# Kernel tuning notes

Measured on AMD Instinct MI355X. Metric: run time of the kernel, lower is better.

Reference implementation:

```python
import jax, jax.numpy as jnp
import numpy as np

B, T, I, H = 256, 2048, 12, 64


def setup_inputs() -> dict:
    key = jax.random.key(0)
    ks = jax.random.split(key, 7)
    s_ih = 1.0 / np.sqrt(H)
    return {
        "x": jax.random.normal(ks[0], (B, T, I), dtype=jnp.float32),
        "w_ih": jax.random.uniform(ks[1], (4 * H, I), minval=-s_ih, maxval=s_ih, dtype=jnp.float32),
        "w_hh": jax.random.uniform(ks[2], (4 * H, H), minval=-s_ih, maxval=s_ih, dtype=jnp.float32),
        "b_ih": jax.random.uniform(ks[3], (4 * H,), minval=-s_ih, maxval=s_ih, dtype=jnp.float32),
        "b_hh": jax.random.uniform(ks[4], (4 * H,), minval=-s_ih, maxval=s_ih, dtype=jnp.float32),
        "fc_w": jax.random.uniform(ks[5], (1, H), minval=-s_ih, maxval=s_ih, dtype=jnp.float32),
        "fc_b": jax.random.uniform(ks[6], (1,), minval=-s_ih, maxval=s_ih, dtype=jnp.float32),
    }


def _lstm(x, w_ih, w_hh, b_ih, b_hh):
    # Precompute input projections for all timesteps: [B,T,4H]
    gx = jnp.einsum("bti,gi->btg", x, w_ih) + b_ih + b_hh
    gx = jnp.swapaxes(gx, 0, 1)  # [T,B,4H] for scan over time
    h0 = jnp.zeros((x.shape[0], w_hh.shape[1]), dtype=x.dtype)
    c0 = jnp.zeros_like(h0)
    Hd = w_hh.shape[1]

    def step(carry, g_t):
        h, c = carry
        gates = g_t + h @ w_hh.T  # [B,4H]
        i = jax.nn.sigmoid(gates[:, 0 * Hd:1 * Hd])
        f = jax.nn.sigmoid(gates[:, 1 * Hd:2 * Hd])
        g = jnp.tanh(gates[:, 2 * Hd:3 * Hd])
        o = jax.nn.sigmoid(gates[:, 3 * Hd:4 * Hd])
        c_new = f * c + i * g
        h_new = o * jnp.tanh(c_new)
        return (h_new, c_new), h_new

    _, hs = jax.lax.scan(step, (h0, c0), gx)  # hs: [T,B,H]
    return jnp.swapaxes(hs, 0, 1)  # [B,T,H]


def reference(x, w_ih, w_hh, b_ih, b_hh, fc_w, fc_b):
    out = _lstm(x, w_ih, w_hh, b_ih, b_hh)            # [B,T,H]
    return jnp.einsum("bth,oh->bto", out, fc_w) + fc_b  # [B,T,1]
```

## Files before the change

### kernel.cpp

```cpp
#include <hip/hip_runtime.h>

constexpr int Bn = 256;
constexpr int Tn = 2048;
constexpr int In = 12;
constexpr int Hn = 64;
constexpr int TCH = 512;
constexpr int CHUNK = 16;

constexpr float LOG2E = 1.44269504088896340736f;

__device__ __forceinline__ float frcp(float v) { return __builtin_amdgcn_rcpf(v); }

template <int CTRL>
__device__ __forceinline__ float dppq(float v) {
    int i = __float_as_int(v);
    i = __builtin_amdgcn_mov_dpp(i, CTRL, 0xF, 0xF, false);
    return __int_as_float(i);
}
__device__ __forceinline__ float rdl(float v, int l) {
    return __int_as_float(__builtin_amdgcn_readlane(__float_as_int(v), l));
}

extern "C" __global__ void __launch_bounds__(256, 1)
lstm_fused_kernel(const float* __restrict__ x,
                  const float* __restrict__ w_ih,
                  const float* __restrict__ w_hh,
                  const float* __restrict__ b_ih,
                  const float* __restrict__ b_hh,
                  const float* __restrict__ fc_w,
                  const float* __restrict__ fc_b,
                  float* __restrict__ out)
{
    __shared__ __align__(16) float xbuf[TCH * 16];
    __shared__ __align__(16) float pbuf[2][4][256];
    __shared__ __align__(16) float hist[CHUNK][Hn];

    const int tid  = threadIdx.x;
    const int lane = tid & 63;
    const int w    = tid >> 6;
    const int g    = lane & 3;
    const int i16  = lane >> 2;
    const int jown = 16 * w + i16;
    const int ro   = 64 * g + jown;
    const int b    = blockIdx.x;

    const int wbase = ((lane >> 2) & 3) * 64 + (lane >> 4) * 16 + 4 * (lane & 3);
    const int rbase = w * 64 + g * 16 + i16;

    const float4* xsrc4 = (const float4*)(x + (size_t)b * Tn * In);

    #pragma unroll
    for (int k = 0; k < 8; ++k) {
        int idx = tid + k * 256;
        xbuf[(idx >> 2) * 16 + 12 + (idx & 3)] = 0.0f;
    }

    float whh_s[4][16];
    #pragma unroll
    for (int r = 0; r < 4; ++r) {
        const float4* src = (const float4*)(w_hh + (4 * lane + r) * Hn + 16 * w);
        float4 v0 = src[0], v1 = src[1], v2 = src[2], v3 = src[3];
        whh_s[r][0]=v0.x;  whh_s[r][1]=v0.y;  whh_s[r][2]=v0.z;  whh_s[r][3]=v0.w;
        whh_s[r][4]=v1.x;  whh_s[r][5]=v1.y;  whh_s[r][6]=v1.z;  whh_s[r][7]=v1.w;
        whh_s[r][8]=v2.x;  whh_s[r][9]=v2.y;  whh_s[r][10]=v2.z; whh_s[r][11]=v2.w;
        whh_s[r][12]=v3.x; whh_s[r][13]=v3.y; whh_s[r][14]=v3.z; whh_s[r][15]=v3.w;
    }
    #pragma unroll
    for (int r = 0; r < 4; ++r)
        #pragma unroll
        for (int k = 0; k < 16; k += 4)
            asm volatile("" : "+v"(whh_s[r][k+0]), "+v"(whh_s[r][k+1]),
                              "+v"(whh_s[r][k+2]), "+v"(whh_s[r][k+3]));

    float wih_s[4][4];
    if (w < 3) {
        #pragma unroll
        for (int r = 0; r < 4; ++r) {
            float4 v = *(const float4*)(w_ih + (4 * lane + r) * In + 4 * w);
            wih_s[r][0]=v.x; wih_s[r][1]=v.y; wih_s[r][2]=v.z; wih_s[r][3]=v.w;
        }
    } else {
        #pragma unroll
        for (int r = 0; r < 4; ++r)
            wih_s[r][0]=wih_s[r][1]=wih_s[r][2]=wih_s[r][3]=0.0f;
    }
    #pragma unroll
    for (int r = 0; r < 4; ++r)
        asm volatile("" : "+v"(wih_s[r][0]), "+v"(wih_s[r][1]),
                          "+v"(wih_s[r][2]), "+v"(wih_s[r][3]));

    const float bias = b_ih[ro] + b_hh[ro];
    const float m    = (g == 2) ? 2.0f : 1.0f;
    const float madd = (g == 2) ? -1.0f : 0.0f;
    const float me   = (g == 2) ? (-2.0f * LOG2E) : (-LOG2E);
    const int   fq   = tid & 15;
    const int   fs   = tid >> 4;
    const float4 fw4 = *(const float4*)(fc_w + 4 * fq);
    const float fcb  = fc_b[0];

    float h_own = 0.0f;
    float c     = 0.0f;

    float* outb = out + (size_t)b * Tn;

    for (int ci = 0; ci < Tn / CHUNK; ++ci) {
        const int T0 = ci * CHUNK;

        if ((T0 & (TCH - 1)) == 0) {
            const int qtr = T0 >> 9;
            #pragma unroll
            for (int k = 0; k < 6; ++k) {
                int li  = tid + k * 256;
                int t_l = li / 3;
                int i4  = li % 3;
                ((float4*)xbuf)[t_l * 4 + i4] = xsrc4[qtr * 1536 + li];
            }
            __syncthreads();
        }

        #pragma unroll
        for (int s = 0; s < CHUNK; ++s) {
            const int tl = (T0 + s) & (TCH - 1);

            float hs0  = rdl(h_own,  0), hs1  = rdl(h_own,  4);
            float hs2  = rdl(h_own,  8), hs3  = rdl(h_own, 12);
            float hs4  = rdl(h_own, 16), hs5  = rdl(h_own, 20);
            float hs6  = rdl(h_own, 24), hs7  = rdl(h_own, 28);
            float hs8  = rdl(h_own, 32), hs9  = rdl(h_own, 36);
            float hs10 = rdl(h_own, 40), hs11 = rdl(h_own, 44);
            float hs12 = rdl(h_own, 48), hs13 = rdl(h_own, 52);
            float hs14 = rdl(h_own, 56), hs15 = rdl(h_own, 60);

            const float4 xv = *(const float4*)(xbuf + tl * 16 + 4 * w);
            float p0 = hs0 * whh_s[0][0], p1 = hs0 * whh_s[1][0];
            float p2 = hs0 * whh_s[2][0], p3 = hs0 * whh_s[3][0];
            #define HFMA(K, HS) \
                p0 = fmaf(HS, whh_s[0][K], p0);  p1 = fmaf(HS, whh_s[1][K], p1); \
                p2 = fmaf(HS, whh_s[2][K], p2);  p3 = fmaf(HS, whh_s[3][K], p3);
            HFMA(1,  hs1)  HFMA(2,  hs2)  HFMA(3,  hs3)
            HFMA(4,  hs4)  HFMA(5,  hs5)  HFMA(6,  hs6)  HFMA(7,  hs7)
            HFMA(8,  hs8)  HFMA(9,  hs9)  HFMA(10, hs10) HFMA(11, hs11)
            HFMA(12, hs12) HFMA(13, hs13) HFMA(14, hs14) HFMA(15, hs15)
            #undef HFMA
            p0 = fmaf(xv.x, wih_s[0][0], p0);  p1 = fmaf(xv.x, wih_s[1][0], p1);
            p2 = fmaf(xv.x, wih_s[2][0], p2);  p3 = fmaf(xv.x, wih_s[3][0], p3);
            p0 = fmaf(xv.y, wih_s[0][1], p0);  p1 = fmaf(xv.y, wih_s[1][1], p1);
            p2 = fmaf(xv.y, wih_s[2][1], p2);  p3 = fmaf(xv.y, wih_s[3][1], p3);
            p0 = fmaf(xv.z, wih_s[0][2], p0);  p1 = fmaf(xv.z, wih_s[1][2], p1);
            p2 = fmaf(xv.z, wih_s[2][2], p2);  p3 = fmaf(xv.z, wih_s[3][2], p3);
            p0 = fmaf(xv.w, wih_s[0][3], p0);  p1 = fmaf(xv.w, wih_s[1][3], p1);
            p2 = fmaf(xv.w, wih_s[2][3], p2);  p3 = fmaf(xv.w, wih_s[3][3], p3);

            float4 pv; pv.x = p0; pv.y = p1; pv.z = p2; pv.w = p3;
            *(float4*)(&pbuf[s & 1][w][wbase]) = pv;
            __syncthreads();

            const float* pb = &pbuf[s & 1][0][0];
            float a = ((pb[rbase] + pb[256 + rbase]) +
                       (pb[512 + rbase] + pb[768 + rbase])) + bias;
            float e   = exp2f(me * a);
            float act = fmaf(m, frcp(1.0f + e), madd);

            float iv = dppq<0x00>(act);
            float fv = dppq<0x55>(act);
            float gv = dppq<0xAA>(act);
            float ov = dppq<0xFF>(act);

            c = fmaf(fv, c, iv * gv);
            float e2 = exp2f(-2.0f * LOG2E * c);
            h_own = ov * fmaf(2.0f, frcp(1.0f + e2), -1.0f);

            if (g == 0) hist[s][jown] = h_own;
        }

        __syncthreads();
        {
            const float4 hv = *(const float4*)(&hist[fs][4 * fq]);
            float pp = hv.x * fw4.x + hv.y * fw4.y + hv.z * fw4.z + hv.w * fw4.w;
            #pragma unroll
            for (int off = 8; off; off >>= 1)
                pp += __shfl_xor(pp, off, 16);
            if (fq == 0) outb[T0 + fs] = pp + fcb;
        }
    }
}

extern "C" void kernel_launch(void* const* d_in, const int* in_sizes, int n_in,
                              void* d_out, int out_size, void* d_ws, size_t ws_size,
                              hipStream_t stream) {
    const float* x    = (const float*)d_in[0];
    const float* w_ih = (const float*)d_in[1];
    const float* w_hh = (const float*)d_in[2];
    const float* b_ih = (const float*)d_in[3];
    const float* b_hh = (const float*)d_in[4];
    const float* fc_w = (const float*)d_in[5];
    const float* fc_b = (const float*)d_in[6];
    float* out = (float*)d_out;

    lstm_fused_kernel<<<Bn, 256, 0, stream>>>(x, w_ih, w_hh, b_ih, b_hh,
                                              fc_w, fc_b, out);
}
```

Measured before the change: 713.9 us.

## Split LSTM recurrent matvec across eight waves with 512-thread blocks

Doubles the block size to 512 threads, so each of the eight waves handles an 8-column slice of the hidden state instead of a 16-column slice. This halves the per-step readlane broadcasts and the FMA chain on the serial recurrence path. In exchange, the cross-wave reduction now sums eight partials instead of four, using a padded shared buffer. The per-step barrier also spans eight waves, and half of each wave's lanes redundantly compute the gate activations.

```diff
diff --git a/kernel.cpp b/kernel.cpp
--- a/kernel.cpp
+++ b/kernel.cpp
@@ -21,7 +21,7 @@
     return __int_as_float(__builtin_amdgcn_readlane(__float_as_int(v), l));
 }
 
-extern "C" __global__ void __launch_bounds__(256, 1)
+extern "C" __global__ void __launch_bounds__(512, 1)
 lstm_fused_kernel(const float* __restrict__ x,
                   const float* __restrict__ w_ih,
                   const float* __restrict__ w_hh,
@@ -32,69 +32,62 @@
                   float* __restrict__ out)
 {
     __shared__ __align__(16) float xbuf[TCH * 16];
-    __shared__ __align__(16) float pbuf[2][4][256];
+    __shared__ __align__(16) float pbuf[2][8][288];
     __shared__ __align__(16) float hist[CHUNK][Hn];
 
     const int tid  = threadIdx.x;
     const int lane = tid & 63;
     const int w    = tid >> 6;
-    const int g    = lane & 3;
-    const int i16  = lane >> 2;
-    const int jown = 16 * w + i16;
+    const int lh   = lane & 31;
+    const int g    = lh & 3;
+    const int i8   = lh >> 2;
+    const int jown = 8 * w + i8;
     const int ro   = 64 * g + jown;
     const int b    = blockIdx.x;
 
-    const int wbase = ((lane >> 2) & 3) * 64 + (lane >> 4) * 16 + 4 * (lane & 3);
-    const int rbase = w * 64 + g * 16 + i16;
-
     const float4* xsrc4 = (const float4*)(x + (size_t)b * Tn * In);
 
+    {
+        float4 z; z.x = z.y = z.z = z.w = 0.0f;
+        ((float4*)xbuf)[tid * 4 + 3] = z;
+    }
+
+    float whh_s[4][8];
     #pragma unroll
-    for (int k = 0; k < 8; ++k) {
-        int idx = tid + k * 256;
-        xbuf[(idx >> 2) * 16 + 12 + (idx & 3)] = 0.0f;
-    }
-
-    float whh_s[4][16];
+    for (int mm = 0; mm < 4; ++mm) {
+        const float4* src = (const float4*)(w_hh + (64 * mm + lane) * Hn + 8 * w);
+        float4 v0 = src[0], v1 = src[1];
+        whh_s[mm][0]=v0.x; whh_s[mm][1]=v0.y; whh_s[mm][2]=v0.z; whh_s[mm][3]=v0.w;
+        whh_s[mm][4]=v1.x; whh_s[mm][5]=v1.y; whh_s[mm][6]=v1.z; whh_s[mm][7]=v1.w;
+    }
     #pragma unroll
-    for (int r = 0; r < 4; ++r) {
-        const float4* src = (const float4*)(w_hh + (4 * lane + r) * Hn + 16 * w);
-        float4 v0 = src[0], v1 = src[1], v2 = src[2], v3 = src[3];
-        whh_s[r][0]=v0.x;  whh_s[r][1]=v0.y;  whh_s[r][2]=v0.z;  whh_s[r][3]=v0.w;
-        whh_s[r][4]=v1.x;  whh_s[r][5]=v1.y;  whh_s[r][6]=v1.z;  whh_s[r][7]=v1.w;
-        whh_s[r][8]=v2.x;  whh_s[r][9]=v2.y;  whh_s[r][10]=v2.z; whh_s[r][11]=v2.w;
-        whh_s[r][12]=v3.x; whh_s[r][13]=v3.y; whh_s[r][14]=v3.z; whh_s[r][15]=v3.w;
+    for (int mm = 0; mm < 4; ++mm)
+        #pragma unroll
+        for (int k = 0; k < 8; k += 4)
+            asm volatile("" : "+v"(whh_s[mm][k+0]), "+v"(whh_s[mm][k+1]),
+                              "+v"(whh_s[mm][k+2]), "+v"(whh_s[mm][k+3]));
+
+    float wih_s[4][2];
+    if (w < 6) {
+        #pragma unroll
+        for (int mm = 0; mm < 4; ++mm) {
+            float2 v = *(const float2*)(w_ih + (64 * mm + lane) * In + 2 * w);
+            wih_s[mm][0] = v.x; wih_s[mm][1] = v.y;
+        }
+    } else {
+        #pragma unroll
+        for (int mm = 0; mm < 4; ++mm) { wih_s[mm][0] = 0.0f; wih_s[mm][1] = 0.0f; }
     }
     #pragma unroll
-    for (int r = 0; r < 4; ++r)
-        #pragma unroll
-        for (int k = 0; k < 16; k += 4)
-            asm volatile("" : "+v"(whh_s[r][k+0]), "+v"(whh_s[r][k+1]),
-                              "+v"(whh_s[r][k+2]), "+v"(whh_s[r][k+3]));
-
-    float wih_s[4][4];
-    if (w < 3) {
-        #pragma unroll
-        for (int r = 0; r < 4; ++r) {
-            float4 v = *(const float4*)(w_ih + (4 * lane + r) * In + 4 * w);
-            wih_s[r][0]=v.x; wih_s[r][1]=v.y; wih_s[r][2]=v.z; wih_s[r][3]=v.w;
-        }
-    } else {
-        #pragma unroll
-        for (int r = 0; r < 4; ++r)
-            wih_s[r][0]=wih_s[r][1]=wih_s[r][2]=wih_s[r][3]=0.0f;
-    }
-    #pragma unroll
-    for (int r = 0; r < 4; ++r)
-        asm volatile("" : "+v"(wih_s[r][0]), "+v"(wih_s[r][1]),
-                          "+v"(wih_s[r][2]), "+v"(wih_s[r][3]));
+    for (int mm = 0; mm < 4; ++mm)
+        asm volatile("" : "+v"(wih_s[mm][0]), "+v"(wih_s[mm][1]));
 
     const float bias = b_ih[ro] + b_hh[ro];
-    const float m    = (g == 2) ? 2.0f : 1.0f;
-    const float madd = (g == 2) ? -1.0f : 0.0f;
+    const float scl  = (g == 2) ? 2.0f : 1.0f;
+    const float soff = (g == 2) ? -1.0f : 0.0f;
     const float me   = (g == 2) ? (-2.0f * LOG2E) : (-LOG2E);
     const int   fq   = tid & 15;
-    const int   fs   = tid >> 4;
+    const int   fs   = (tid >> 4) & 15;
     const float4 fw4 = *(const float4*)(fc_w + 4 * fq);
     const float fcb  = fc_b[0];
 
@@ -109,8 +102,8 @@
         if ((T0 & (TCH - 1)) == 0) {
             const int qtr = T0 >> 9;
             #pragma unroll
-            for (int k = 0; k < 6; ++k) {
-                int li  = tid + k * 256;
+            for (int k = 0; k < 3; ++k) {
+                int li  = tid + k * 512;
                 int t_l = li / 3;
                 int i4  = li % 3;
                 ((float4*)xbuf)[t_l * 4 + i4] = xsrc4[qtr * 1536 + li];
@@ -122,59 +115,66 @@
         for (int s = 0; s < CHUNK; ++s) {
             const int tl = (T0 + s) & (TCH - 1);
 
-            float hs0  = rdl(h_own,  0), hs1  = rdl(h_own,  4);
-            float hs2  = rdl(h_own,  8), hs3  = rdl(h_own, 12);
-            float hs4  = rdl(h_own, 16), hs5  = rdl(h_own, 20);
-            float hs6  = rdl(h_own, 24), hs7  = rdl(h_own, 28);
-            float hs8  = rdl(h_own, 32), hs9  = rdl(h_own, 36);
-            float hs10 = rdl(h_own, 40), hs11 = rdl(h_own, 44);
-            float hs12 = rdl(h_own, 48), hs13 = rdl(h_own, 52);
-            float hs14 = rdl(h_own, 56), hs15 = rdl(h_own, 60);
-
-            const float4 xv = *(const float4*)(xbuf + tl * 16 + 4 * w);
+            float2 xv;
+            xv.x = 0.0f; xv.y = 0.0f;
+            if (w < 6) xv = *(const float2*)(xbuf + tl * 16 + 2 * w);
+
+            float hs0 = rdl(h_own,  0), hs1 = rdl(h_own,  4);
+            float hs2 = rdl(h_own,  8), hs3 = rdl(h_own, 12);
+            float hs4 = rdl(h_own, 16), hs5 = rdl(h_own, 20);
+            float hs6 = rdl(h_own, 24), hs7 = rdl(h_own, 28);
+
             float p0 = hs0 * whh_s[0][0], p1 = hs0 * whh_s[1][0];
             float p2 = hs0 * whh_s[2][0], p3 = hs0 * whh_s[3][0];
             #define HFMA(K, HS) \
                 p0 = fmaf(HS, whh_s[0][K], p0);  p1 = fmaf(HS, whh_s[1][K], p1); \
                 p2 = fmaf(HS, whh_s[2][K], p2);  p3 = fmaf(HS, whh_s[3][K], p3);
-            HFMA(1,  hs1)  HFMA(2,  hs2)  HFMA(3,  hs3)
-            HFMA(4,  hs4)  HFMA(5,  hs5)  HFMA(6,  hs6)  HFMA(7,  hs7)
-            HFMA(8,  hs8)  HFMA(9,  hs9)  HFMA(10, hs10) HFMA(11, hs11)
-            HFMA(12, hs12) HFMA(13, hs13) HFMA(14, hs14) HFMA(15, hs15)
+            HFMA(1, hs1) HFMA(2, hs2) HFMA(3, hs3)
+            HFMA(4, hs4) HFMA(5, hs5) HFMA(6, hs6) HFMA(7, hs7)
             #undef HFMA
-            p0 = fmaf(xv.x, wih_s[0][0], p0);  p1 = fmaf(xv.x, wih_s[1][0], p1);
-            p2 = fmaf(xv.x, wih_s[2][0], p2);  p3 = fmaf(xv.x, wih_s[3][0], p3);
-            p0 = fmaf(xv.y, wih_s[0][1], p0);  p1 = fmaf(xv.y, wih_s[1][1], p1);
-            p2 = fmaf(xv.y, wih_s[2][1], p2);  p3 = fmaf(xv.y, wih_s[3][1], p3);
-            p0 = fmaf(xv.z, wih_s[0][2], p0);  p1 = fmaf(xv.z, wih_s[1][2], p1);
-            p2 = fmaf(xv.z, wih_s[2][2], p2);  p3 = fmaf(xv.z, wih_s[3][2], p3);
-            p0 = fmaf(xv.w, wih_s[0][3], p0);  p1 = fmaf(xv.w, wih_s[1][3], p1);
-            p2 = fmaf(xv.w, wih_s[2][3], p2);  p3 = fmaf(xv.w, wih_s[3][3], p3);
-
-            float4 pv; pv.x = p0; pv.y = p1; pv.z = p2; pv.w = p3;
-            *(float4*)(&pbuf[s & 1][w][wbase]) = pv;
+            if (w < 6) {
+                p0 = fmaf(xv.x, wih_s[0][0], p0);  p1 = fmaf(xv.x, wih_s[1][0], p1);
+                p2 = fmaf(xv.x, wih_s[2][0], p2);  p3 = fmaf(xv.x, wih_s[3][0], p3);
+                p0 = fmaf(xv.y, wih_s[0][1], p0);  p1 = fmaf(xv.y, wih_s[1][1], p1);
+                p2 = fmaf(xv.y, wih_s[2][1], p2);  p3 = fmaf(xv.y, wih_s[3][1], p3);
+            }
+
+            {
+                float* pw = &pbuf[s & 1][w][0];
+                pw[lane]       = p0;
+                pw[72 + lane]  = p1;
+                pw[144 + lane] = p2;
+                pw[216 + lane] = p3;
+            }
             __syncthreads();
 
-            const float* pb = &pbuf[s & 1][0][0];
-            float a = ((pb[rbase] + pb[256 + rbase]) +
-                       (pb[512 + rbase] + pb[768 + rbase])) + bias;
-            float e   = exp2f(me * a);
-            float act = fmaf(m, frcp(1.0f + e), madd);
-
-            float iv = dppq<0x00>(act);
-            float fv = dppq<0x55>(act);
-            float gv = dppq<0xAA>(act);
-            float ov = dppq<0xFF>(act);
-
-            c = fmaf(fv, c, iv * gv);
-            float e2 = exp2f(-2.0f * LOG2E * c);
-            h_own = ov * fmaf(2.0f, frcp(1.0f + e2), -1.0f);
-
-            if (g == 0) hist[s][jown] = h_own;
+            {
+                const float* pr = &pbuf[s & 1][0][0];
+                const int rb = 72 * g + jown;
+                float q0 = pr[rb],            q1 = pr[288  + rb];
+                float q2 = pr[576 + rb],      q3 = pr[864  + rb];
+                float q4 = pr[1152 + rb],     q5 = pr[1440 + rb];
+                float q6 = pr[1728 + rb],     q7 = pr[2016 + rb];
+                float a = (((q0 + q1) + (q2 + q3)) + ((q4 + q5) + (q6 + q7))) + bias;
+
+                float e   = exp2f(me * a);
+                float act = fmaf(scl, frcp(1.0f + e), soff);
+
+                float iv = dppq<0x00>(act);
+                float fv = dppq<0x55>(act);
+                float gv = dppq<0xAA>(act);
+                float ov = dppq<0xFF>(act);
+
+                c = fmaf(fv, c, iv * gv);
+                float e2 = exp2f(-2.0f * LOG2E * c);
+                h_own = ov * fmaf(2.0f, frcp(1.0f + e2), -1.0f);
+
+                if (g == 0 && lane < 32) hist[s][jown] = h_own;
+            }
         }
 
         __syncthreads();
-        {
+        if (tid < 256) {
             const float4 hv = *(const float4*)(&hist[fs][4 * fq]);
             float pp = hv.x * fw4.x + hv.y * fw4.y + hv.z * fw4.z + hv.w * fw4.w;
             #pragma unroll
@@ -197,6 +197,6 @@
     const float* fc_b = (const float*)d_in[6];
     float* out = (float*)d_out;
 
-    lstm_fused_kernel<<<Bn, 256, 0, stream>>>(x, w_ih, w_hh, b_ih, b_hh,
+    lstm_fused_kernel<<<Bn, 512, 0, stream>>>(x, w_ih, w_hh, b_ih, b_hh,
                                               fc_w, fc_b, out);
 }
```

New measurement: 840.0 us. 1.18x slower.

## Pack two batch chains per 512-thread block with shared barriers

Applied to the files above, without the earlier changes.

Each block now runs two independent LSTM batch chains (512 threads), halving the grid to 128 blocks. Each chain gets its own slice of x, partial-sum and history buffers, and the x staging tile shrinks to 256 timesteps. The intent is to interleave two latency-bound recurrences on one compute unit to hide step latency. The risk is that half the CUs sit idle and every per-step barrier now synchronizes twice as many waves.

```diff
diff --git a/kernel.cpp b/kernel.cpp
--- a/kernel.cpp
+++ b/kernel.cpp
@@ -4,8 +4,12 @@
 constexpr int Tn = 2048;
 constexpr int In = 12;
 constexpr int Hn = 64;
-constexpr int TCH = 512;
+constexpr int TCH = 256;
 constexpr int CHUNK = 16;
+
+constexpr int XBUF = TCH * 16;
+constexpr int PBUF = 2 * 4 * 256;
+constexpr int HIST = CHUNK * Hn;
 
 constexpr float LOG2E = 1.44269504088896340736f;
 
@@ -21,7 +25,7 @@
     return __int_as_float(__builtin_amdgcn_readlane(__float_as_int(v), l));
 }
 
-extern "C" __global__ void __launch_bounds__(256, 1)
+extern "C" __global__ void __launch_bounds__(512, 1)
 lstm_fused_kernel(const float* __restrict__ x,
                   const float* __restrict__ w_ih,
                   const float* __restrict__ w_hh,
@@ -31,29 +35,31 @@
                   const float* __restrict__ fc_b,
                   float* __restrict__ out)
 {
-    __shared__ __align__(16) float xbuf[TCH * 16];
-    __shared__ __align__(16) float pbuf[2][4][256];
-    __shared__ __align__(16) float hist[CHUNK][Hn];
-
-    const int tid  = threadIdx.x;
-    const int lane = tid & 63;
-    const int w    = tid >> 6;
-    const int g    = lane & 3;
-    const int i16  = lane >> 2;
-    const int jown = 16 * w + i16;
-    const int ro   = 64 * g + jown;
-    const int b    = blockIdx.x;
+    __shared__ __align__(16) float xbuf[2 * XBUF];
+    __shared__ __align__(16) float pbuf[2 * PBUF];
+    __shared__ __align__(16) float hist[2 * HIST];
+
+    const int tid   = threadIdx.x;
+    const int chain = tid >> 8;
+    const int lt    = tid & 255;
+    const int lane  = lt & 63;
+    const int w     = lt >> 6;
+    const int g     = lane & 3;
+    const int i16   = lane >> 2;
+    const int jown  = 16 * w + i16;
+    const int ro    = 64 * g + jown;
+    const int b     = 2 * blockIdx.x + chain;
 
     const int wbase = ((lane >> 2) & 3) * 64 + (lane >> 4) * 16 + 4 * (lane & 3);
     const int rbase = w * 64 + g * 16 + i16;
 
+    float* xb  = xbuf + chain * XBUF;
+    float* pb2 = pbuf + chain * PBUF;
+    float* hb  = hist + chain * HIST;
+
     const float4* xsrc4 = (const float4*)(x + (size_t)b * Tn * In);
 
-    #pragma unroll
-    for (int k = 0; k < 8; ++k) {
-        int idx = tid + k * 256;
-        xbuf[(idx >> 2) * 16 + 12 + (idx & 3)] = 0.0f;
-    }
+    ((float4*)xb)[lt * 4 + 3] = float4{0.f, 0.f, 0.f, 0.f};
 
     float whh_s[4][16];
     #pragma unroll
@@ -90,11 +96,11 @@
                           "+v"(wih_s[r][2]), "+v"(wih_s[r][3]));
 
     const float bias = b_ih[ro] + b_hh[ro];
-    const float m    = (g == 2) ? 2.0f : 1.0f;
-    const float madd = (g == 2) ? -1.0f : 0.0f;
+    const float scl  = (g == 2) ? 2.0f : 1.0f;
+    const float soff = (g == 2) ? -1.0f : 0.0f;
     const float me   = (g == 2) ? (-2.0f * LOG2E) : (-LOG2E);
-    const int   fq   = tid & 15;
-    const int   fs   = tid >> 4;
+    const int   fq   = lt & 15;
+    const int   fs   = lt >> 4;
     const float4 fw4 = *(const float4*)(fc_w + 4 * fq);
     const float fcb  = fc_b[0];
 
@@ -107,13 +113,13 @@
         const int T0 = ci * CHUNK;
 
         if ((T0 & (TCH - 1)) == 0) {
-            const int qtr = T0 >> 9;
+            const int qtr = T0 >> 8;
             #pragma unroll
-            for (int k = 0; k < 6; ++k) {
-                int li  = tid + k * 256;
+            for (int k = 0; k < 3; ++k) {
+                int li  = lt + k * 256;
                 int t_l = li / 3;
                 int i4  = li % 3;
-                ((float4*)xbuf)[t_l * 4 + i4] = xsrc4[qtr * 1536 + li];
+                ((float4*)xb)[t_l * 4 + i4] = xsrc4[qtr * 768 + li];
             }
             __syncthreads();
         }
@@ -131,7 +137,7 @@
             float hs12 = rdl(h_own, 48), hs13 = rdl(h_own, 52);
             float hs14 = rdl(h_own, 56), hs15 = rdl(h_own, 60);
 
-            const float4 xv = *(const float4*)(xbuf + tl * 16 + 4 * w);
+            const float4 xv = *(const float4*)(xb + tl * 16 + 4 * w);
             float p0 = hs0 * whh_s[0][0], p1 = hs0 * whh_s[1][0];
             float p2 = hs0 * whh_s[2][0], p3 = hs0 * whh_s[3][0];
             #define HFMA(K, HS) \
@@ -152,14 +158,14 @@
             p2 = fmaf(xv.w, wih_s[2][3], p2);  p3 = fmaf(xv.w, wih_s[3][3], p3);
 
             float4 pv; pv.x = p0; pv.y = p1; pv.z = p2; pv.w = p3;
-            *(float4*)(&pbuf[s & 1][w][wbase]) = pv;
+            *(float4*)(pb2 + (s & 1) * 1024 + w * 256 + wbase) = pv;
             __syncthreads();
 
-            const float* pb = &pbuf[s & 1][0][0];
-            float a = ((pb[rbase] + pb[256 + rbase]) +
-                       (pb[512 + rbase] + pb[768 + rbase])) + bias;
+            const float* pr = pb2 + (s & 1) * 1024;
+            float a = ((pr[rbase] + pr[256 + rbase]) +
+                       (pr[512 + rbase] + pr[768 + rbase])) + bias;
             float e   = exp2f(me * a);
-            float act = fmaf(m, frcp(1.0f + e), madd);
+            float act = fmaf(scl, frcp(1.0f + e), soff);
 
             float iv = dppq<0x00>(act);
             float fv = dppq<0x55>(act);
@@ -170,12 +176,12 @@
             float e2 = exp2f(-2.0f * LOG2E * c);
             h_own = ov * fmaf(2.0f, frcp(1.0f + e2), -1.0f);
 
-            if (g == 0) hist[s][jown] = h_own;
+            if (g == 0) hb[s * Hn + jown] = h_own;
         }
 
         __syncthreads();
         {
-            const float4 hv = *(const float4*)(&hist[fs][4 * fq]);
+            const float4 hv = *(const float4*)(hb + fs * Hn + 4 * fq);
             float pp = hv.x * fw4.x + hv.y * fw4.y + hv.z * fw4.z + hv.w * fw4.w;
             #pragma unroll
             for (int off = 8; off; off >>= 1)
@@ -197,6 +203,6 @@
     const float* fc_b = (const float*)d_in[6];
     float* out = (float*)d_out;
 
-    lstm_fused_kernel<<<Bn, 256, 0, stream>>>(x, w_ih, w_hh, b_ih, b_hh,
-                                              fc_w, fc_b, out);
-}
+    lstm_fused_kernel<<<Bn / 2, 512, 0, stream>>>(x, w_ih, w_hh, b_ih, b_hh,
+                                                  fc_w, fc_b, out);
+}
```

Result: slower. 994.0 us (+39.2%).
